# Kernel tuning notes

Hardware: AMD Instinct MI355X
Metric: run time of the kernel (lower is better)

The kernel has to match this reference:

```python
import jax, jax.numpy as jnp
import numpy as np

B, S, D, H, F, R = 4, 128, 512, 8, 2048, 8
DH = D // H
THRESH = 0.1  # hardcoded in the torch module


def _ln(x, g, b):
    m = x.mean(-1, keepdims=True)
    v = ((x - m) ** 2).mean(-1, keepdims=True)
    return (x - m) * jax.lax.rsqrt(v + 1e-5) * g + b


def setup_inputs() -> dict:
    key = jax.random.key(0)
    ks = jax.random.split(key, 12)
    w = lambda k, shape, std: jax.random.normal(k, shape, jnp.float32) * std
    s = 1.0 / np.sqrt(D)
    qk_std = 2.0 / np.sqrt(D)  # peaky attention so adjacency threshold fires
    return {
        "x": jax.random.normal(ks[0], (B, S, D), jnp.float32),
        "ln1_g": jnp.ones(D, jnp.float32), "ln1_b": jnp.zeros(D, jnp.float32),
        "wq": w(ks[1], (D, D), qk_std), "bq": jnp.zeros(D, jnp.float32),
        "wk": w(ks[2], (D, D), qk_std), "bk": jnp.zeros(D, jnp.float32),
        "wv": w(ks[3], (D, D), s), "bv": jnp.zeros(D, jnp.float32),
        "wo": w(ks[4], (D, D), s), "bo": jnp.zeros(D, jnp.float32),
        "w1": w(ks[5], (D, F), s), "b1": jnp.zeros(F, jnp.float32),
        "w2": w(ks[6], (F, D), 1.0 / np.sqrt(F)), "b2": jnp.zeros(D, jnp.float32),
        "rc_w1": w(ks[7], (2 * D, D), 1.0 / np.sqrt(2 * D)), "rc_b1": jnp.zeros(D, jnp.float32),
        "rc_w2": w(ks[8], (D, R), s), "rc_b2": jnp.zeros(R, jnp.float32),
        "kg_w": w(ks[9], (R, D, D), s),
        "s2n_w": w(ks[10], (D, D), s), "s2n_b": jnp.zeros(D, jnp.float32),
        "ln2_g": jnp.ones(D, jnp.float32), "ln2_b": jnp.zeros(D, jnp.float32),
    }


def reference(x, ln1_g, ln1_b, wq, bq, wk, bk, wv, bv, wo, bo,
              w1, b1, w2, b2, rc_w1, rc_b1, rc_w2, rc_b2,
              kg_w, s2n_w, s2n_b, ln2_g, ln2_b):
    # pre-norm attention
    xn = _ln(x, ln1_g, ln1_b)
    q = (xn @ wq + bq).reshape(B, S, H, DH)
    k = (xn @ wk + bk).reshape(B, S, H, DH)
    v = (xn @ wv + bv).reshape(B, S, H, DH)
    scores = jnp.einsum('bihd,bjhd->bhij', q, k) / np.sqrt(DH)
    attn = jax.nn.softmax(scores, axis=-1)                  # [B,H,S,S]
    ctx = jnp.einsum('bhij,bjhd->bihd', attn, v).reshape(B, S, D)
    attn_out = ctx @ wo + bo
    # FFN -> neural_understanding (no residual, as in source)
    nu = jax.nn.relu(attn_out @ w1 + b1) @ w2 + b2          # [B,S,D]
    # dynamic edge extraction, expressed as a dense mask (jit-safe)
    am = attn.mean(axis=1)                                  # [B,S,S]
    adj = (am > THRESH) & (~jnp.eye(S, dtype=bool))         # u != v
    # relation classifier on every (u,v) pair; mask selects real edges
    a_part = nu @ rc_w1[:D]                                 # concept1 half
    b_part = nu @ rc_w1[D:]                                 # concept2 half
    h = jax.nn.relu(a_part[:, :, None, :] + b_part[:, None, :, :] + rc_b1)  # [B,S,S,D]
    logits = h @ rc_w2 + rc_b2                              # [B,S,S,R]
    pred = jnp.argmax(logits, axis=-1)
    valid = adj & (pred != 0)                               # relation 0 == NONE
    oh = jax.nn.one_hot(pred, R, dtype=nu.dtype) * valid[..., None].astype(nu.dtype)
    # RGCN-style knowledge graph conv: message u -> v with per-relation weight
    transformed = jnp.einsum('bud,rde->bure', nu, kg_w)     # [B,S,R,D]
    agg = jnp.einsum('buvr,bure->bve', oh, transformed)     # [B,S,D]
    reasoned = nu + agg
    neural_result = reasoned @ s2n_w + s2n_b
    out = _ln(x + neural_result, ln2_g, ln2_b)
    return out
```

## Files before the change

### kernel.cpp

```cpp
#include <hip/hip_runtime.h>
#include <hip/hip_bf16.h>

#define B_ 4
#define S_ 128
#define D_ 512
#define H_ 8
#define DH_ 64
#define F_ 2048
#define R_ 8
#define BS_ (B_ * S_)
#define BSD_ (BS_ * D_)
#define E_ 262144

typedef __attribute__((ext_vector_type(8))) short short8;
typedef __attribute__((ext_vector_type(4))) float f32x4;
typedef __attribute__((ext_vector_type(4))) unsigned short ushort4v;

__device__ __forceinline__ void split2(float a, unsigned short& h, unsigned short& l) {
    unsigned u = __float_as_uint(a);
    unsigned hr = (u + 0x7FFFu + ((u >> 16) & 1u)) >> 16;
    h = (unsigned short)hr;
    float lo = a - __uint_as_float(hr << 16);
    unsigned u2 = __float_as_uint(lo);
    l = (unsigned short)((u2 + 0x7FFFu + ((u2 >> 16) & 1u)) >> 16);
}

struct TDesc { const float* s; unsigned short* h; unsigned short* l; int K; int N; int off; };
struct TPack { TDesc d[10]; };

__global__ void prep_kernel(TPack p, int nt, const float* __restrict__ x,
                            const float* __restrict__ g, const float* __restrict__ be,
                            unsigned short* __restrict__ xh, unsigned short* __restrict__ xl,
                            int* __restrict__ ecount) {
    __shared__ float tr[32][33];
    __shared__ float red[256];
    int bid = blockIdx.x;
    if (bid == 0 && threadIdx.x == 0) *ecount = 0;
    if (bid < nt) {
        int wi = 0;
#pragma unroll
        for (int i = 1; i < 10; ++i) if (bid >= p.d[i].off) wi = i;
        const TDesc dd = p.d[wi];
        int t = bid - dd.off;
        int ntk = dd.K / 32;
        int tk = t % ntk, tn = t / ntk;
        int k0 = tk * 32, n0 = tn * 32;
        int col = threadIdx.x & 31, rg = threadIdx.x >> 5;
#pragma unroll
        for (int i = 0; i < 4; ++i) {
            int row = rg * 4 + i;
            tr[row][col] = dd.s[(size_t)(k0 + row) * dd.N + n0 + col];
        }
        __syncthreads();
#pragma unroll
        for (int i = 0; i < 4; ++i) {
            int n = n0 + rg * 4 + i;
            int k = k0 + col;
            unsigned short h, l;
            split2(tr[col][rg * 4 + i], h, l);
            dd.h[(size_t)n * dd.K + k] = h;
            dd.l[(size_t)n * dd.K + k] = l;
        }
    } else {
        int row = bid - nt;
        int t = threadIdx.x;
        const float* xr = x + (size_t)row * D_;
        float v0 = xr[t], v1 = xr[t + 256];
        red[t] = v0 + v1;
        __syncthreads();
        for (int off = 128; off > 0; off >>= 1) { if (t < off) red[t] += red[t + off]; __syncthreads(); }
        float mean = red[0] * (1.0f / D_);
        __syncthreads();
        float d0 = v0 - mean, d1 = v1 - mean;
        red[t] = d0 * d0 + d1 * d1;
        __syncthreads();
        for (int off = 128; off > 0; off >>= 1) { if (t < off) red[t] += red[t + off]; __syncthreads(); }
        float rs = rsqrtf(red[0] * (1.0f / D_) + 1e-5f);
        float o0 = d0 * rs * g[t] + be[t];
        float o1 = d1 * rs * g[t + 256] + be[t + 256];
        unsigned short h, l;
        split2(o0, h, l); xh[(size_t)row * D_ + t] = h;       xl[(size_t)row * D_ + t] = l;
        split2(o1, h, l); xh[(size_t)row * D_ + t + 256] = h; xl[(size_t)row * D_ + t + 256] = l;
    }
}

struct GemmLds {
    unsigned short A[2][2][64][64];
    unsigned short B[2][2][64][64];
};

__device__ __forceinline__ void gload16(const unsigned short* g, unsigned short* l) {
    __builtin_amdgcn_global_load_lds(
        (const __attribute__((address_space(1))) void*)g,
        (__attribute__((address_space(3))) void*)l, 16, 0, 0);
}

__device__ __forceinline__ void mgemm_core(const unsigned short* __restrict__ Ath,
                                           const unsigned short* __restrict__ Atl,
                                           const unsigned short* __restrict__ Bth,
                                           const unsigned short* __restrict__ Btl,
                                           int K, int rowBase, int colBase,
                                           int kStart, int nsteps,
                                           f32x4 acc[2][2], GemmLds* L) {
    int tid = threadIdx.x;
    int w = tid >> 6, lane = tid & 63;
    int lm = lane & 15, quad = lane >> 4;
    int wm = (w & 1) * 32, wn = (w >> 1) * 32;
    int r0 = w * 8 + (lane >> 3);
    int lc = ((lane & 7) ^ (lane >> 3)) * 8;
    int wb = w * 512;
    size_t a0 = (size_t)(rowBase + r0) * K + kStart + lc;
    size_t a1 = (size_t)(rowBase + r0 + 32) * K + kStart + lc;
    size_t b0 = (size_t)(colBase + r0) * K + kStart + lc;
    size_t b1 = (size_t)(colBase + r0 + 32) * K + kStart + lc;
    unsigned short* AB = &L->A[0][0][0][0];
    unsigned short* BB = &L->B[0][0][0][0];
    auto stage = [&](int p, size_t koff) {
        gload16(&Ath[a0 + koff], AB + p * 8192 + wb);
        gload16(&Ath[a1 + koff], AB + p * 8192 + 2048 + wb);
        gload16(&Atl[a0 + koff], AB + p * 8192 + 4096 + wb);
        gload16(&Atl[a1 + koff], AB + p * 8192 + 6144 + wb);
        gload16(&Bth[b0 + koff], BB + p * 8192 + wb);
        gload16(&Bth[b1 + koff], BB + p * 8192 + 2048 + wb);
        gload16(&Btl[b0 + koff], BB + p * 8192 + 4096 + wb);
        gload16(&Btl[b1 + koff], BB + p * 8192 + 6144 + wb);
    };
    stage(0, 0);
    __syncthreads();
    for (int s = 0; s < nsteps; ++s) {
        int p = s & 1;
        if (s + 1 < nsteps) stage(p ^ 1, (size_t)(s + 1) * 64);
#pragma unroll
        for (int sub = 0; sub < 2; ++sub) {
            short8 ah[2], al[2], bh[2], bl[2];
            int pc = ((sub * 4 + quad) ^ (lm & 7)) * 8;
#pragma unroll
            for (int t = 0; t < 2; ++t) {
                int ra = (wm + t * 16 + lm) * 64 + pc;
                int rb = (wn + t * 16 + lm) * 64 + pc;
                ah[t] = *(const short8*)(AB + p * 8192 + ra);
                al[t] = *(const short8*)(AB + p * 8192 + 4096 + ra);
                bh[t] = *(const short8*)(BB + p * 8192 + rb);
                bl[t] = *(const short8*)(BB + p * 8192 + 4096 + rb);
            }
#pragma unroll
            for (int tm = 0; tm < 2; ++tm)
#pragma unroll
                for (int tn = 0; tn < 2; ++tn) {
                    acc[tm][tn] = __builtin_amdgcn_mfma_f32_16x16x32_bf16(ah[tm], bh[tn], acc[tm][tn], 0, 0, 0);
                    acc[tm][tn] = __builtin_amdgcn_mfma_f32_16x16x32_bf16(ah[tm], bl[tn], acc[tm][tn], 0, 0, 0);
                    acc[tm][tn] = __builtin_amdgcn_mfma_f32_16x16x32_bf16(al[tm], bh[tn], acc[tm][tn], 0, 0, 0);
                }
        }
        __syncthreads();
    }
}

__device__ __forceinline__ void gemm_epilogue(f32x4 acc[2][2], const float* bias,
                                              float* Cf, unsigned short* Ch, unsigned short* Cl,
                                              int N, int relu, int rowBase, int colBase) {
    int tid = threadIdx.x;
    int w = tid >> 6, lane = tid & 63;
    int lm = lane & 15, quad = lane >> 4;
    int wm = (w & 1) * 32, wn = (w >> 1) * 32;
#pragma unroll
    for (int tm = 0; tm < 2; ++tm)
#pragma unroll
        for (int tn = 0; tn < 2; ++tn) {
            int col = colBase + wn + tn * 16 + lm;
            float bi = bias ? bias[col] : 0.f;
#pragma unroll
            for (int r = 0; r < 4; ++r) {
                int row = rowBase + wm + tm * 16 + quad * 4 + r;
                float v = acc[tm][tn][r] + bi;
                if (relu) v = fmaxf(v, 0.f);
                size_t o = (size_t)row * N + col;
                if (Cf) Cf[o] = v;
                if (Ch) {
                    unsigned short sh, sl;
                    split2(v, sh, sl);
                    Ch[o] = sh; Cl[o] = sl;
                }
            }
        }
}

__global__ __launch_bounds__(256) void mgemm_kernel(const unsigned short* __restrict__ Ath,
                                                    const unsigned short* __restrict__ Atl,
                                                    const unsigned short* __restrict__ Bth,
                                                    const unsigned short* __restrict__ Btl,
                                                    const float* __restrict__ bias,
                                                    float* __restrict__ Cf,
                                                    unsigned short* __restrict__ Ch,
                                                    unsigned short* __restrict__ Cl,
                                                    int N, int K, int relu) {
    __shared__ GemmLds L;
    int rowBase = blockIdx.y * 64, colBase = blockIdx.x * 64;
    f32x4 acc[2][2] = {};
    mgemm_core(Ath, Atl, Bth, Btl, K, rowBase, colBase, 0, K / 64, acc, &L);
    gemm_epilogue(acc, bias, Cf, Ch, Cl, N, relu, rowBase, colBase);
}

__global__ __launch_bounds__(256) void mgemm_zw_kernel(const unsigned short* __restrict__ Ath,
                                                       const unsigned short* __restrict__ Atl,
                                                       const unsigned short* __restrict__ Bth,
                                                       const unsigned short* __restrict__ Btl,
                                                       const float* __restrict__ b0,
                                                       const float* __restrict__ b1,
                                                       const float* __restrict__ b2,
                                                       float* __restrict__ Cbase,
                                                       int M, int N, int K) {
    __shared__ GemmLds L;
    int z = blockIdx.z;
    const unsigned short* bth = Bth + (size_t)z * K * N;
    const unsigned short* btl = Btl + (size_t)z * K * N;
    const float* bias = (z == 0) ? b0 : (z == 1) ? b1 : b2;
    float* C = Cbase + (size_t)z * M * N;
    int rowBase = blockIdx.y * 64, colBase = blockIdx.x * 64;
    f32x4 acc[2][2] = {};
    mgemm_core(Ath, Atl, bth, btl, K, rowBase, colBase, 0, K / 64, acc, &L);
    gemm_epilogue(acc, bias, C, nullptr, nullptr, N, 0, rowBase, colBase);
}

__global__ __launch_bounds__(256) void mgemm_part_kernel(const unsigned short* __restrict__ Ath,
                                                         const unsigned short* __restrict__ Atl,
                                                         const unsigned short* __restrict__ Bth,
                                                         const unsigned short* __restrict__ Btl,
                                                         float* __restrict__ Cbase,
                                                         int M, int N, int K) {
    __shared__ GemmLds L;
    int ks = gridDim.z, z = blockIdx.z;
    int kLen = K / ks, kStart = z * kLen;
    float* C = Cbase + (size_t)z * M * N;
    int rowBase = blockIdx.y * 64, colBase = blockIdx.x * 64;
    f32x4 acc[2][2] = {};
    mgemm_core(Ath, Atl, Bth, Btl, K, rowBase, colBase, kStart, kLen / 64, acc, &L);
    gemm_epilogue(acc, nullptr, C, nullptr, nullptr, N, 0, rowBase, colBase);
}

__global__ __launch_bounds__(256) void wo_adj_kernel(const unsigned short* __restrict__ Ath,
                                                     const unsigned short* __restrict__ Atl,
                                                     const unsigned short* __restrict__ Bth,
                                                     const unsigned short* __restrict__ Btl,
                                                     const float* __restrict__ bias,
                                                     unsigned short* __restrict__ Ch,
                                                     unsigned short* __restrict__ Cl,
                                                     const float* __restrict__ attnP,
                                                     int* __restrict__ ecount,
                                                     int* __restrict__ elist,
                                                     int* __restrict__ rel) {
    __shared__ GemmLds L;
    int bid = blockIdx.x;
    if (bid < 64) {
        int rowBase = (bid >> 3) * 64, colBase = (bid & 7) * 64;
        f32x4 acc[2][2] = {};
        mgemm_core(Ath, Atl, Bth, Btl, D_, rowBase, colBase, 0, D_ / 64, acc, &L);
        gemm_epilogue(acc, bias, nullptr, Ch, Cl, D_, 0, rowBase, colBase);
    } else {
        int idx = (bid - 64) * 256 + threadIdx.x;
        int j = idx & (S_ - 1);
        int bi = idx >> 7;
        int i = bi & (S_ - 1);
        int b = bi >> 7;
        float s = 0.f;
#pragma unroll
        for (int h = 0; h < H_; ++h) s += attnP[(((size_t)(b * H_ + h)) * S_ + i) * S_ + j];
        s *= (1.0f / H_);
        rel[idx] = 0;
        if (s > 0.1f && i != j) {
            int p = atomicAdd(ecount, 1);
            elist[p] = idx;
        }
    }
}

__global__ void reduce4_kernel(const float* __restrict__ part, const float* __restrict__ b2,
                               float* __restrict__ nu,
                               unsigned short* __restrict__ nh, unsigned short* __restrict__ nl) {
    int base = blockIdx.x * 1024 + threadIdx.x * 4;
    f32x4 s = *(const f32x4*)&b2[base & (D_ - 1)];
#pragma unroll
    for (int z = 0; z < 4; ++z) s += *(const f32x4*)&part[(size_t)z * BSD_ + base];
    *(f32x4*)&nu[base] = s;
    ushort4v hv, lv;
#pragma unroll
    for (int i = 0; i < 4; ++i) { unsigned short h, l; split2(s[i], h, l); hv[i] = h; lv[i] = l; }
    *(ushort4v*)&nh[base] = hv;
    *(ushort4v*)&nl[base] = lv;
}

__global__ void reduce8_kernel(const float* __restrict__ part, const float* __restrict__ nu,
                               unsigned short* __restrict__ rh, unsigned short* __restrict__ rl) {
    int base = blockIdx.x * 1024 + threadIdx.x * 4;
    f32x4 s = *(const f32x4*)&nu[base];
#pragma unroll
    for (int z = 0; z < 8; ++z) s += *(const f32x4*)&part[(size_t)z * BSD_ + base];
    ushort4v hv, lv;
#pragma unroll
    for (int i = 0; i < 4; ++i) { unsigned short h, l; split2(s[i], h, l); hv[i] = h; lv[i] = l; }
    *(ushort4v*)&rh[base] = hv;
    *(ushort4v*)&rl[base] = lv;
}

__global__ __launch_bounds__(512) void attn_kernel2(const float* __restrict__ q,
                                                    const float* __restrict__ k,
                                                    const float* __restrict__ v,
                                                    float* __restrict__ attnP,
                                                    unsigned short* __restrict__ ch,
                                                    unsigned short* __restrict__ cl) {
    __shared__ float ksm[S_][DH_ + 3];
    __shared__ float qsm[16][DH_];
    __shared__ float psm[16][S_];
    int tid = threadIdx.x;
    int w = tid >> 6, lane = tid & 63;
    int blk = blockIdx.x;
    int ig = blk & 7;
    int bh = blk >> 3;
    int h = bh & (H_ - 1);
    int b = bh >> 3;
    int i0 = ig * 16;
    const float* kb = k + (size_t)b * S_ * D_ + h * DH_;
    for (int j = w; j < S_; j += 8) ksm[j][lane] = kb[(size_t)j * D_ + lane];
    for (int il = w; il < 16; il += 8)
        qsm[il][lane] = q[(size_t)(b * S_ + i0 + il) * D_ + h * DH_ + lane];
    __syncthreads();
    const float* vb = v + (size_t)b * S_ * D_ + h * DH_ + lane;
#pragma unroll
    for (int c = 0; c < 2; ++c) {
        int il = w + c * 8;
        int i = i0 + il;
        float s0 = 0.f, s1 = 0.f;
#pragma unroll 8
        for (int d = 0; d < DH_; ++d) {
            float qd = qsm[il][d];
            s0 += qd * ksm[lane][d];
            s1 += qd * ksm[lane + 64][d];
        }
        s0 *= 0.125f; s1 *= 0.125f;
        float m = fmaxf(s0, s1);
#pragma unroll
        for (int off = 32; off > 0; off >>= 1) m = fmaxf(m, __shfl_xor(m, off));
        float e0 = __expf(s0 - m), e1 = __expf(s1 - m);
        float sum = e0 + e1;
#pragma unroll
        for (int off = 32; off > 0; off >>= 1) sum += __shfl_xor(sum, off);
        float inv = 1.f / sum;
        float p0 = e0 * inv, p1 = e1 * inv;
        float* arow = attnP + ((size_t)(b * H_ + h) * S_ + i) * S_;
        arow[lane] = p0;
        arow[lane + 64] = p1;
        psm[il][lane] = p0;
        psm[il][lane + 64] = p1;
        float acc = 0.f;
        for (int j = 0; j < S_; ++j) acc += psm[il][j] * vb[(size_t)j * D_];
        unsigned short sh, sl;
        split2(acc, sh, sl);
        size_t o = (size_t)(b * S_ + i) * D_ + h * DH_ + lane;
        ch[o] = sh; cl[o] = sl;
    }
}

__global__ __launch_bounds__(256) void edge_kernel(const float* __restrict__ a_part,
                                                   const float* __restrict__ b_part,
                                                   const float* __restrict__ rc_b1,
                                                   const float* __restrict__ rc_w2,
                                                   const float* __restrict__ rc_b2,
                                                   const int* __restrict__ elist,
                                                   const int* __restrict__ ecount,
                                                   int* __restrict__ rel) {
    __shared__ float w2t[R_][D_];
    for (int idx = threadIdx.x; idx < R_ * D_; idx += 256)
        w2t[idx & 7][idx >> 3] = rc_w2[idx];
    __syncthreads();
    int w = threadIdx.x >> 6, lane = threadIdx.x & 63;
    int n = *ecount;
    for (int e = blockIdx.x * 4 + w; e < n; e += gridDim.x * 4) {
        int idx = elist[e];
        int vv = idx & (S_ - 1);
        int bu = idx >> 7;
        int u = bu & (S_ - 1);
        int b = bu >> 7;
        const float* ap = a_part + (size_t)(b * S_ + u) * D_;
        const float* bp = b_part + (size_t)(b * S_ + vv) * D_;
        float lp[R_];
#pragma unroll
        for (int r = 0; r < R_; ++r) lp[r] = 0.f;
#pragma unroll
        for (int jj = 0; jj < D_ / 64; ++jj) {
            int d = lane + jj * 64;
            float hv = fmaxf(ap[d] + bp[d] + rc_b1[d], 0.f);
#pragma unroll
            for (int r = 0; r < R_; ++r) lp[r] += hv * w2t[r][d];
        }
#pragma unroll
        for (int r = 0; r < R_; ++r) {
#pragma unroll
            for (int off = 32; off > 0; off >>= 1) lp[r] += __shfl_down(lp[r], off);
        }
        if (lane == 0) {
            float best = lp[0] + rc_b2[0];
            int bi = 0;
#pragma unroll
            for (int r = 1; r < R_; ++r) {
                float L = lp[r] + rc_b2[r];
                if (L > best) { best = L; bi = r; }
            }
            rel[idx] = bi;
        }
    }
}

__global__ __launch_bounds__(128) void mbuild_kernel(const float* __restrict__ nu,
                                                     const int* __restrict__ rel,
                                                     unsigned short* __restrict__ Mh,
                                                     unsigned short* __restrict__ Ml) {
    __shared__ float acc[R_ * D_];
    __shared__ int rl[S_];
    int blk = blockIdx.x;
    int vv = blk & (S_ - 1);
    int b = blk >> 7;
    int t = threadIdx.x;
    for (int i = t; i < R_ * D_; i += 128) acc[i] = 0.f;
    rl[t] = rel[((size_t)b * S_ + t) * S_ + vv];
    __syncthreads();
    for (int u = 0; u < S_; ++u) {
        int r = rl[u];
        if (r > 0) {
            const float* nurow = nu + (size_t)(b * S_ + u) * D_;
            float* arow = acc + r * D_;
#pragma unroll
            for (int jj = 0; jj < D_ / 128; ++jj) arow[t + jj * 128] += nurow[t + jj * 128];
        }
    }
    __syncthreads();
    unsigned short* Hrow = Mh + (size_t)blk * (R_ * D_);
    unsigned short* Lrow = Ml + (size_t)blk * (R_ * D_);
    for (int i = t; i < R_ * D_; i += 128) {
        unsigned short sh, sl;
        split2(acc[i], sh, sl);
        Hrow[i] = sh; Lrow[i] = sl;
    }
}

__global__ void ln2_kernel(const float* __restrict__ x, const float* __restrict__ y,
                           const float* __restrict__ g, const float* __restrict__ be,
                           float* __restrict__ out) {
    int row = blockIdx.x;
    int t = threadIdx.x;
    __shared__ float red[256];
    float v0 = x[row * D_ + t]       + y[row * D_ + t];
    float v1 = x[row * D_ + t + 256] + y[row * D_ + t + 256];
    red[t] = v0 + v1;
    __syncthreads();
    for (int off = 128; off > 0; off >>= 1) {
        if (t < off) red[t] += red[t + off];
        __syncthreads();
    }
    float mean = red[0] * (1.0f / D_);
    __syncthreads();
    float d0 = v0 - mean, d1 = v1 - mean;
    red[t] = d0 * d0 + d1 * d1;
    __syncthreads();
    for (int off = 128; off > 0; off >>= 1) {
        if (t < off) red[t] += red[t + off];
        __syncthreads();
    }
    float rs = rsqrtf(red[0] * (1.0f / D_) + 1e-5f);
    out[row * D_ + t]       = d0 * rs * g[t]       + be[t];
    out[row * D_ + t + 256] = d1 * rs * g[t + 256] + be[t + 256];
}

extern "C" void kernel_launch(void* const* d_in, const int* in_sizes, int n_in,
                              void* d_out, int out_size, void* d_ws, size_t ws_size,
                              hipStream_t stream) {
    const float* x     = (const float*)d_in[0];
    const float* ln1_g = (const float*)d_in[1];
    const float* ln1_b = (const float*)d_in[2];
    const float* wq    = (const float*)d_in[3];
    const float* bq    = (const float*)d_in[4];
    const float* wk    = (const float*)d_in[5];
    const float* bk    = (const float*)d_in[6];
    const float* wv    = (const float*)d_in[7];
    const float* bv    = (const float*)d_in[8];
    const float* wo    = (const float*)d_in[9];
    const float* bo    = (const float*)d_in[10];
    const float* w1    = (const float*)d_in[11];
    const float* b1    = (const float*)d_in[12];
    const float* w2    = (const float*)d_in[13];
    const float* b2    = (const float*)d_in[14];
    const float* rc_w1 = (const float*)d_in[15];
    const float* rc_b1 = (const float*)d_in[16];
    const float* rc_w2 = (const float*)d_in[17];
    const float* rc_b2 = (const float*)d_in[18];
    const float* kg_w  = (const float*)d_in[19];
    const float* s2n_w = (const float*)d_in[20];
    const float* s2n_b = (const float*)d_in[21];
    const float* ln2_g = (const float*)d_in[22];
    const float* ln2_b = (const float*)d_in[23];
    float* out = (float*)d_out;

    const int BS  = BS_;
    const int BSD = BSD_;

    unsigned short* wt = (unsigned short*)d_ws;
    unsigned short* qkv_h = wt;
    unsigned short* qkv_l = wt + 3 * E_;
    unsigned short* wo_h  = wt + 6 * E_;
    unsigned short* wo_l  = wt + 7 * E_;
    unsigned short* w1_h  = wt + 8 * E_;
    unsigned short* w1_l  = wt + 12 * E_;
    unsigned short* w2_h  = wt + 16 * E_;
    unsigned short* w2_l  = wt + 20 * E_;
    unsigned short* rc_h  = wt + 24 * E_;
    unsigned short* rc_l  = wt + 26 * E_;
    unsigned short* kg_h  = wt + 28 * E_;
    unsigned short* kg_l  = wt + 36 * E_;
    unsigned short* s2_h  = wt + 44 * E_;
    unsigned short* s2_l  = wt + 45 * E_;

    unsigned short* xn_h  = wt + 46 * E_;
    unsigned short* xn_l  = xn_h + BSD;
    unsigned short* ctx_h = xn_l + BSD;
    unsigned short* ctx_l = ctx_h + BSD;
    unsigned short* ao_h  = ctx_l + BSD;
    unsigned short* ao_l  = ao_h + BSD;
    unsigned short* hid_h = ao_l + BSD;
    unsigned short* hid_l = hid_h + (size_t)BS * F_;
    unsigned short* nu_h  = hid_l + (size_t)BS * F_;
    unsigned short* nu_l  = nu_h + BSD;
    unsigned short* mb_h  = nu_l + BSD;
    unsigned short* mb_l  = mb_h + (size_t)BS * R_ * D_;
    unsigned short* rs_h  = mb_l + (size_t)BS * R_ * D_;
    unsigned short* rs_l  = rs_h + BSD;

    float* fbase  = (float*)(rs_l + BSD);
    float* q      = fbase;
    float* v_     = q + 2 * BSD;
    float* apart  = q + 3 * BSD;
    float* nu     = apart + 2 * BSD;
    float* y      = nu + BSD;
    float* part4  = y + BSD;
    float* part8  = part4 + 4 * BSD;
    float* attnP  = part8 + 8 * BSD;

    int* rel    = (int*)(attnP + 2097152);
    int* ecount = rel + B_ * S_ * S_;
    int* elist  = ecount + 64;

    TPack tp;
    int off = 0;
    auto setd = [&](int i, const float* s, unsigned short* h, unsigned short* l, int K, int N) {
        tp.d[i] = TDesc{s, h, l, K, N, off};
        off += (K / 32) * (N / 32);
    };
    setd(0, wq, qkv_h,          qkv_l,          D_, D_);
    setd(1, wk, qkv_h + E_,     qkv_l + E_,     D_, D_);
    setd(2, wv, qkv_h + 2 * E_, qkv_l + 2 * E_, D_, D_);
    setd(3, wo, wo_h, wo_l, D_, D_);
    setd(4, w1, w1_h, w1_l, D_, F_);
    setd(5, w2, w2_h, w2_l, F_, D_);
    setd(6, rc_w1,            rc_h,      rc_l,      D_, D_);
    setd(7, rc_w1 + D_ * D_,  rc_h + E_, rc_l + E_, D_, D_);
    setd(8, kg_w, kg_h, kg_l, R_ * D_, D_);
    setd(9, s2n_w, s2_h, s2_l, D_, D_);
    hipLaunchKernelGGL(prep_kernel, dim3(off + BS), dim3(256), 0, stream, tp, off,
                       x, ln1_g, ln1_b, xn_h, xn_l, ecount);

    hipLaunchKernelGGL(mgemm_zw_kernel, dim3(D_ / 64, BS / 64, 3), dim3(256), 0, stream,
                       xn_h, xn_l, qkv_h, qkv_l, bq, bk, bv, q, BS, D_, D_);
    hipLaunchKernelGGL(attn_kernel2, dim3(B_ * H_ * 8), dim3(512), 0, stream,
                       q, q + BSD, v_, attnP, ctx_h, ctx_l);
    hipLaunchKernelGGL(wo_adj_kernel, dim3(64 + 256), dim3(256), 0, stream,
                       ctx_h, ctx_l, wo_h, wo_l, bo, ao_h, ao_l, attnP, ecount, elist, rel);
    hipLaunchKernelGGL(mgemm_kernel, dim3(F_ / 64, BS / 64), dim3(256), 0, stream,
                       ao_h, ao_l, w1_h, w1_l, b1, (float*)nullptr, hid_h, hid_l, F_, D_, 1);
    hipLaunchKernelGGL(mgemm_part_kernel, dim3(D_ / 64, BS / 64, 4), dim3(256), 0, stream,
                       hid_h, hid_l, w2_h, w2_l, part4, BS, D_, F_);
    hipLaunchKernelGGL(reduce4_kernel, dim3(BSD / 1024), dim3(256), 0, stream,
                       part4, b2, nu, nu_h, nu_l);
    hipLaunchKernelGGL(mgemm_zw_kernel, dim3(D_ / 64, BS / 64, 2), dim3(256), 0, stream,
                       nu_h, nu_l, rc_h, rc_l, (const float*)nullptr, (const float*)nullptr,
                       (const float*)nullptr, apart, BS, D_, D_);
    hipLaunchKernelGGL(edge_kernel, dim3(256), dim3(256), 0, stream,
                       apart, apart + BSD, rc_b1, rc_w2, rc_b2, elist, ecount, rel);
    hipLaunchKernelGGL(mbuild_kernel, dim3(BS), dim3(128), 0, stream, nu, rel, mb_h, mb_l);
    hipLaunchKernelGGL(mgemm_part_kernel, dim3(D_ / 64, BS / 64, 8), dim3(256), 0, stream,
                       mb_h, mb_l, kg_h, kg_l, part8, BS, D_, R_ * D_);
    hipLaunchKernelGGL(reduce8_kernel, dim3(BSD / 1024), dim3(256), 0, stream,
                       part8, nu, rs_h, rs_l);
    hipLaunchKernelGGL(mgemm_kernel, dim3(D_ / 64, BS / 64), dim3(256), 0, stream,
                       rs_h, rs_l, s2_h, s2_l, s2n_b, y, (unsigned short*)nullptr,
                       (unsigned short*)nullptr, D_, D_, 0);
    hipLaunchKernelGGL(ln2_kernel, dim3(BS), dim3(256), 0, stream, x, y, ln2_g, ln2_b, out);
}
```

Baseline: 228.1 us.

## Replace atomic edge list with ballot adjacency bitmask and fuse edge classify into mbuild

The adjacency pass now writes a per-row 128-bit bitmask via wave ballot instead of appending edges to a global list with atomics and zeroing a rel array. The separate edge classification and message-build kernels are merged into one 512-thread kernel per target node, which reads the bitmask, classifies the incoming edges, and accumulates messages in LDS. This removes one launch, the atomic contention, and the rel round trip through global memory. The cost is that edge work is no longer load-balanced across blocks, since each block handles a variable number of edges.

```diff
diff --git a/kernel.cpp b/kernel.cpp
--- a/kernel.cpp
+++ b/kernel.cpp
@@ -30,12 +30,10 @@
 
 __global__ void prep_kernel(TPack p, int nt, const float* __restrict__ x,
                             const float* __restrict__ g, const float* __restrict__ be,
-                            unsigned short* __restrict__ xh, unsigned short* __restrict__ xl,
-                            int* __restrict__ ecount) {
+                            unsigned short* __restrict__ xh, unsigned short* __restrict__ xl) {
     __shared__ float tr[32][33];
     __shared__ float red[256];
     int bid = blockIdx.x;
-    if (bid == 0 && threadIdx.x == 0) *ecount = 0;
     if (bid < nt) {
         int wi = 0;
 #pragma unroll
@@ -246,9 +244,7 @@
                                                      unsigned short* __restrict__ Ch,
                                                      unsigned short* __restrict__ Cl,
                                                      const float* __restrict__ attnP,
-                                                     int* __restrict__ ecount,
-                                                     int* __restrict__ elist,
-                                                     int* __restrict__ rel) {
+                                                     unsigned long long* __restrict__ adjm) {
     __shared__ GemmLds L;
     int bid = blockIdx.x;
     if (bid < 64) {
@@ -266,11 +262,10 @@
 #pragma unroll
         for (int h = 0; h < H_; ++h) s += attnP[(((size_t)(b * H_ + h)) * S_ + i) * S_ + j];
         s *= (1.0f / H_);
-        rel[idx] = 0;
-        if (s > 0.1f && i != j) {
-            int p = atomicAdd(ecount, 1);
-            elist[p] = idx;
-        }
+        int pred = (s > 0.1f && i != j) ? 1 : 0;
+        unsigned long long m = __ballot(pred);
+        if ((threadIdx.x & 63) == 0)
+            adjm[(size_t)bi * 2 + ((threadIdx.x >> 6) & 1)] = m;
     }
 }
 
@@ -360,82 +355,73 @@
     }
 }
 
-__global__ __launch_bounds__(256) void edge_kernel(const float* __restrict__ a_part,
-                                                   const float* __restrict__ b_part,
-                                                   const float* __restrict__ rc_b1,
-                                                   const float* __restrict__ rc_w2,
-                                                   const float* __restrict__ rc_b2,
-                                                   const int* __restrict__ elist,
-                                                   const int* __restrict__ ecount,
-                                                   int* __restrict__ rel) {
+__global__ __launch_bounds__(512) void mbuild_edge_kernel(const float* __restrict__ nu,
+                                                          const float* __restrict__ a_part,
+                                                          const float* __restrict__ b_part,
+                                                          const float* __restrict__ rc_b1,
+                                                          const float* __restrict__ rc_w2,
+                                                          const float* __restrict__ rc_b2,
+                                                          const unsigned long long* __restrict__ adjm,
+                                                          unsigned short* __restrict__ Mh,
+                                                          unsigned short* __restrict__ Ml) {
+    __shared__ float acc[R_ * D_];
     __shared__ float w2t[R_][D_];
-    for (int idx = threadIdx.x; idx < R_ * D_; idx += 256)
-        w2t[idx & 7][idx >> 3] = rc_w2[idx];
-    __syncthreads();
-    int w = threadIdx.x >> 6, lane = threadIdx.x & 63;
-    int n = *ecount;
-    for (int e = blockIdx.x * 4 + w; e < n; e += gridDim.x * 4) {
-        int idx = elist[e];
-        int vv = idx & (S_ - 1);
-        int bu = idx >> 7;
-        int u = bu & (S_ - 1);
-        int b = bu >> 7;
-        const float* ap = a_part + (size_t)(b * S_ + u) * D_;
-        const float* bp = b_part + (size_t)(b * S_ + vv) * D_;
-        float lp[R_];
-#pragma unroll
-        for (int r = 0; r < R_; ++r) lp[r] = 0.f;
-#pragma unroll
-        for (int jj = 0; jj < D_ / 64; ++jj) {
-            int d = lane + jj * 64;
-            float hv = fmaxf(ap[d] + bp[d] + rc_b1[d], 0.f);
-#pragma unroll
-            for (int r = 0; r < R_; ++r) lp[r] += hv * w2t[r][d];
-        }
-#pragma unroll
-        for (int r = 0; r < R_; ++r) {
-#pragma unroll
-            for (int off = 32; off > 0; off >>= 1) lp[r] += __shfl_down(lp[r], off);
-        }
-        if (lane == 0) {
-            float best = lp[0] + rc_b2[0];
-            int bi = 0;
-#pragma unroll
-            for (int r = 1; r < R_; ++r) {
-                float L = lp[r] + rc_b2[r];
-                if (L > best) { best = L; bi = r; }
-            }
-            rel[idx] = bi;
-        }
-    }
-}
-
-__global__ __launch_bounds__(128) void mbuild_kernel(const float* __restrict__ nu,
-                                                     const int* __restrict__ rel,
-                                                     unsigned short* __restrict__ Mh,
-                                                     unsigned short* __restrict__ Ml) {
-    __shared__ float acc[R_ * D_];
+    __shared__ float bsm[D_];
     __shared__ int rl[S_];
     int blk = blockIdx.x;
     int vv = blk & (S_ - 1);
     int b = blk >> 7;
     int t = threadIdx.x;
-    for (int i = t; i < R_ * D_; i += 128) acc[i] = 0.f;
-    rl[t] = rel[((size_t)b * S_ + t) * S_ + vv];
+    int w = t >> 6, lane = t & 63;
+    for (int i = t; i < R_ * D_; i += 512) {
+        w2t[i & 7][i >> 3] = rc_w2[i];
+        acc[i] = 0.f;
+    }
+    bsm[t] = b_part[(size_t)blk * D_ + t];
+    __syncthreads();
+    int wsel = vv >> 6, bsh = vv & 63;
+    for (int u = w; u < S_; u += 8) {
+        unsigned long long word = adjm[((size_t)(b * S_ + u)) * 2 + wsel];
+        if ((word >> bsh) & 1ull) {
+            const float* ap = a_part + (size_t)(b * S_ + u) * D_;
+            float lp[R_];
+#pragma unroll
+            for (int r = 0; r < R_; ++r) lp[r] = 0.f;
+#pragma unroll
+            for (int jj = 0; jj < D_ / 64; ++jj) {
+                int d = lane + jj * 64;
+                float hv = fmaxf(ap[d] + bsm[d] + rc_b1[d], 0.f);
+#pragma unroll
+                for (int r = 0; r < R_; ++r) lp[r] += hv * w2t[r][d];
+            }
+#pragma unroll
+            for (int r = 0; r < R_; ++r) {
+#pragma unroll
+                for (int off = 32; off > 0; off >>= 1) lp[r] += __shfl_down(lp[r], off);
+            }
+            if (lane == 0) {
+                float best = lp[0] + rc_b2[0];
+                int bi = 0;
+#pragma unroll
+                for (int r = 1; r < R_; ++r) {
+                    float L = lp[r] + rc_b2[r];
+                    if (L > best) { best = L; bi = r; }
+                }
+                rl[u] = bi;
+            }
+        } else if (lane == 0) {
+            rl[u] = 0;
+        }
+    }
     __syncthreads();
     for (int u = 0; u < S_; ++u) {
         int r = rl[u];
-        if (r > 0) {
-            const float* nurow = nu + (size_t)(b * S_ + u) * D_;
-            float* arow = acc + r * D_;
-#pragma unroll
-            for (int jj = 0; jj < D_ / 128; ++jj) arow[t + jj * 128] += nurow[t + jj * 128];
-        }
+        if (r > 0) acc[r * D_ + t] += nu[(size_t)(b * S_ + u) * D_ + t];
     }
     __syncthreads();
     unsigned short* Hrow = Mh + (size_t)blk * (R_ * D_);
     unsigned short* Lrow = Ml + (size_t)blk * (R_ * D_);
-    for (int i = t; i < R_ * D_; i += 128) {
+    for (int i = t; i < R_ * D_; i += 512) {
         unsigned short sh, sl;
         split2(acc[i], sh, sl);
         Hrow[i] = sh; Lrow[i] = sl;
@@ -543,9 +529,7 @@
     float* part8  = part4 + 4 * BSD;
     float* attnP  = part8 + 8 * BSD;
 
-    int* rel    = (int*)(attnP + 2097152);
-    int* ecount = rel + B_ * S_ * S_;
-    int* elist  = ecount + 64;
+    unsigned long long* adjm = (unsigned long long*)(attnP + 2097152);
 
     TPack tp;
     int off = 0;
@@ -564,14 +548,14 @@
     setd(8, kg_w, kg_h, kg_l, R_ * D_, D_);
     setd(9, s2n_w, s2_h, s2_l, D_, D_);
     hipLaunchKernelGGL(prep_kernel, dim3(off + BS), dim3(256), 0, stream, tp, off,
-                       x, ln1_g, ln1_b, xn_h, xn_l, ecount);
+                       x, ln1_g, ln1_b, xn_h, xn_l);
 
     hipLaunchKernelGGL(mgemm_zw_kernel, dim3(D_ / 64, BS / 64, 3), dim3(256), 0, stream,
                        xn_h, xn_l, qkv_h, qkv_l, bq, bk, bv, q, BS, D_, D_);
     hipLaunchKernelGGL(attn_kernel2, dim3(B_ * H_ * 8), dim3(512), 0, stream,
                        q, q + BSD, v_, attnP, ctx_h, ctx_l);
     hipLaunchKernelGGL(wo_adj_kernel, dim3(64 + 256), dim3(256), 0, stream,
-                       ctx_h, ctx_l, wo_h, wo_l, bo, ao_h, ao_l, attnP, ecount, elist, rel);
+                       ctx_h, ctx_l, wo_h, wo_l, bo, ao_h, ao_l, attnP, adjm);
     hipLaunchKernelGGL(mgemm_kernel, dim3(F_ / 64, BS / 64), dim3(256), 0, stream,
                        ao_h, ao_l, w1_h, w1_l, b1, (float*)nullptr, hid_h, hid_l, F_, D_, 1);
     hipLaunchKernelGGL(mgemm_part_kernel, dim3(D_ / 64, BS / 64, 4), dim3(256), 0, stream,
@@ -581,9 +565,8 @@
     hipLaunchKernelGGL(mgemm_zw_kernel, dim3(D_ / 64, BS / 64, 2), dim3(256), 0, stream,
                        nu_h, nu_l, rc_h, rc_l, (const float*)nullptr, (const float*)nullptr,
                        (const float*)nullptr, apart, BS, D_, D_);
-    hipLaunchKernelGGL(edge_kernel, dim3(256), dim3(256), 0, stream,
-                       apart, apart + BSD, rc_b1, rc_w2, rc_b2, elist, ecount, rel);
-    hipLaunchKernelGGL(mbuild_kernel, dim3(BS), dim3(128), 0, stream, nu, rel, mb_h, mb_l);
+    hipLaunchKernelGGL(mbuild_edge_kernel, dim3(BS), dim3(512), 0, stream,
+                       nu, apart, apart + BSD, rc_b1, rc_w2, rc_b2, adjm, mb_h, mb_l);
     hipLaunchKernelGGL(mgemm_part_kernel, dim3(D_ / 64, BS / 64, 8), dim3(256), 0, stream,
                        mb_h, mb_l, kg_h, kg_l, part8, BS, D_, R_ * D_);
     hipLaunchKernelGGL(reduce8_kernel, dim3(BSD / 1024), dim3(256), 0, stream,
```

Result: no change. 224.1 us, median of 2 (-1.8%).
